# Kernel optimization log

Measured on AMD Instinct MI355X. Metric: run time of the kernel, lower is better.

The kernel has to match this reference:

```python
import jax, jax.numpy as jnp
import numpy as np

EPS = 1e-16


def setup_inputs() -> dict:
    key = jax.random.key(0)
    k1, k2 = jax.random.split(key)
    N, D = 512, 4096
    a = jax.random.normal(k1, (N, D), dtype=jnp.float32)
    p = jax.random.normal(k2, (N, D), dtype=jnp.float32)
    return {"a": a, "p": p}


def reference(a, p):
    N = a.shape[0]
    # Pairwise squared distances between anchors a and positives p:
    # ||a_i||^2 - 2 a_i . p_j + ||p_j||^2   (diag(a a^T) == row norms)
    dot = jnp.matmul(a, p.T)                       # [N, N]
    sq_a = jnp.sum(a * a, axis=-1)                 # [N]
    sq_p = jnp.sum(p * p, axis=-1)                 # [N]
    d2 = sq_a[:, None] - 2.0 * dot + sq_p[None, :]
    d2 = jnp.maximum(d2, 0.0)                      # distances[distances < 0] = 0
    zero_mask = (d2 == 0.0).astype(d2.dtype)
    dist = (1.0 - zero_mask) * jnp.sqrt(d2 + zero_mask * EPS)  # [N, N]

    # Triplet tensor: loss[a, p, n] = dist[a, p] - dist[a, n]
    triplet = dist[:, :, None] - dist[:, None, :]  # [N, N, N]

    # Validity mask: labels = arange(N) -> valid iff p == anchor and n != anchor
    labels = jnp.arange(N)
    label_eq = labels[:, None] == labels[None, :]  # [N, N]
    mask = label_eq[:, :, None] & (~label_eq[:, None, :])  # [N, N, N]

    triplet = mask.astype(triplet.dtype) * triplet
    triplet = jax.nn.relu(triplet)

    num_positive = jnp.sum(triplet > EPS).astype(triplet.dtype)
    loss = jnp.sum(triplet) / (num_positive + EPS)
    return loss
```

## Files before the change

kernel.cpp:

```cpp
#include <hip/hip_runtime.h>
#include <math.h>

#define PN 512
#define PD 4096

#define KSZ 8
#define KCHUNK (PD / KSZ)
#define BK 64
#define NSTAGE (KCHUNK / BK)

#define F_SA 0
#define F_SP 512
#define F_DD 1024
#define F_SUM 1536
#define F_CNT 1537
#define F_DONE 1538
#define F_TILECNT 1600
#define WS_AH_BYTES 8192
#define WS_PH_BYTES (8192 + 4194304)
#define WS_PART_FLOAT 2099200
#define WS_NEED ((size_t)WS_PART_FLOAT * 4 + (size_t)64 * KSZ * 4096 * 4)

typedef __attribute__((ext_vector_type(8))) short short8;
typedef __attribute__((ext_vector_type(4))) float floatx4;

static __device__ __forceinline__ unsigned short f2bf(float x) {
    unsigned int u = __float_as_uint(x);
    u += 0x7fffu + ((u >> 16) & 1u);
    return (unsigned short)(u >> 16);
}

static __device__ __forceinline__ void load16_lds(const void* gp, void* lp) {
    __builtin_amdgcn_global_load_lds(
        (const __attribute__((address_space(1))) unsigned int*)gp,
        (__attribute__((address_space(3))) unsigned int*)lp,
        16, 0, 0);
}

struct ushort4s { unsigned short x, y, z, w; };

__global__ __launch_bounds__(256) void taw_prep_kernel(
        const float* __restrict__ a, const float* __restrict__ p,
        float* __restrict__ ws) {
    const int i = blockIdx.x;
    const int t = threadIdx.x;
    if (i == 0 && t < 128) ((unsigned int*)ws)[1536 + t] = 0u;
    const float4* a4 = (const float4*)(a + (size_t)i * PD);
    const float4* p4 = (const float4*)(p + (size_t)i * PD);
    unsigned short* ah = (unsigned short*)((char*)ws + WS_AH_BYTES) + (size_t)i * PD;
    unsigned short* ph = (unsigned short*)((char*)ws + WS_PH_BYTES) + (size_t)i * PD;
    float sa = 0.f, sp = 0.f, dp = 0.f;
#pragma unroll
    for (int c = 0; c < 4; ++c) {
        const int e = c * 256 + t;
        float4 av = a4[e];
        float4 pv = p4[e];
        sa += av.x * av.x + av.y * av.y + av.z * av.z + av.w * av.w;
        sp += pv.x * pv.x + pv.y * pv.y + pv.z * pv.z + pv.w * pv.w;
        dp += av.x * pv.x + av.y * pv.y + av.z * pv.z + av.w * pv.w;
        ushort4s ab = {f2bf(av.x), f2bf(av.y), f2bf(av.z), f2bf(av.w)};
        ushort4s pb = {f2bf(pv.x), f2bf(pv.y), f2bf(pv.z), f2bf(pv.w)};
        *(ushort4s*)(ah + (size_t)e * 4) = ab;
        *(ushort4s*)(ph + (size_t)e * 4) = pb;
    }
#pragma unroll
    for (int off = 32; off > 0; off >>= 1) {
        sa += __shfl_down(sa, off, 64);
        sp += __shfl_down(sp, off, 64);
        dp += __shfl_down(dp, off, 64);
    }
    __shared__ float red[3][4];
    const int wave = t >> 6;
    if ((t & 63) == 0) { red[0][wave] = sa; red[1][wave] = sp; red[2][wave] = dp; }
    __syncthreads();
    if (t == 0) {
        sa = red[0][0] + red[0][1] + red[0][2] + red[0][3];
        sp = red[1][0] + red[1][1] + red[1][2] + red[1][3];
        dp = red[2][0] + red[2][1] + red[2][2] + red[2][3];
        float d2 = sa - 2.f * dp + sp;
        d2 = fmaxf(d2, 0.f);
        ws[F_SA + i] = sa;
        ws[F_SP + i] = sp;
        ws[F_DD + i] = (d2 == 0.f) ? 0.f : sqrtf(d2);
    }
}

__global__ __launch_bounds__(256) void taw_fused_kernel(float* __restrict__ ws,
                                                        float* __restrict__ out) {
    __shared__ short lds[2][8][64][8];
    const unsigned short* ah = (const unsigned short*)((const char*)ws + WS_AH_BYTES);
    const unsigned short* ph = (const unsigned short*)((const char*)ws + WS_PH_BYTES);
    const int t = threadIdx.x;
    const int lane = t & 63;
    const int w = t >> 6;
    const int wm = w >> 1, wn = w & 1;
    const int i0 = blockIdx.y * 64;
    const int j0 = blockIdx.x * 64;
    const int tile = blockIdx.y * 8 + blockIdx.x;
    const int kzb = blockIdx.z * KCHUNK;
    unsigned int* wsu = (unsigned int*)ws;

    floatx4 acc[2][2] = {{{0.f, 0.f, 0.f, 0.f}, {0.f, 0.f, 0.f, 0.f}},
                         {{0.f, 0.f, 0.f, 0.f}, {0.f, 0.f, 0.f, 0.f}}};

    for (int st = 0; st < NSTAGE; ++st) {
        const int kb = kzb + st * BK;
        __syncthreads();
#pragma unroll
        for (int q = 0; q < 2; ++q) {
            const int g = 2 * w + q;
            const int row = ((g & 3) << 4) + (lane & 15);
            const int kk = kb + ((((g >> 2) << 2) + (lane >> 4)) << 3);
            load16_lds(ah + (size_t)(i0 + row) * PD + kk, &lds[0][g][0][0]);
            load16_lds(ph + (size_t)(j0 + row) * PD + kk, &lds[1][g][0][0]);
        }
        __syncthreads();
#pragma unroll
        for (int s2 = 0; s2 < 2; ++s2) {
            short8 af0 = *(const short8*)&lds[0][s2 * 4 + wm * 2 + 0][lane][0];
            short8 af1 = *(const short8*)&lds[0][s2 * 4 + wm * 2 + 1][lane][0];
            short8 bf0 = *(const short8*)&lds[1][s2 * 4 + wn * 2 + 0][lane][0];
            short8 bf1 = *(const short8*)&lds[1][s2 * 4 + wn * 2 + 1][lane][0];
            acc[0][0] = __builtin_amdgcn_mfma_f32_16x16x32_bf16(af0, bf0, acc[0][0], 0, 0, 0);
            acc[0][1] = __builtin_amdgcn_mfma_f32_16x16x32_bf16(af0, bf1, acc[0][1], 0, 0, 0);
            acc[1][0] = __builtin_amdgcn_mfma_f32_16x16x32_bf16(af1, bf0, acc[1][0], 0, 0, 0);
            acc[1][1] = __builtin_amdgcn_mfma_f32_16x16x32_bf16(af1, bf1, acc[1][1], 0, 0, 0);
        }
    }

    float* part = ws + WS_PART_FLOAT + ((size_t)tile * KSZ + blockIdx.z) * 4096;
    const int jj = wn * 32 + (lane & 15);
    const int ib = wm * 32 + ((lane >> 4) << 2);
#pragma unroll
    for (int rm = 0; rm < 2; ++rm)
#pragma unroll
        for (int rn = 0; rn < 2; ++rn)
#pragma unroll
            for (int r = 0; r < 4; ++r)
                part[(ib + rm * 16 + r) * 64 + jj + rn * 16] = acc[rm][rn][r];

    __syncthreads();
    __shared__ unsigned int lastflag;
    if (t == 0) {
        __threadfence();
        lastflag = (atomicAdd(&wsu[F_TILECNT + tile], 1u) == KSZ - 1) ? 1u : 0u;
    }
    __syncthreads();
    if (!lastflag) return;

    const float* pbase = ws + WS_PART_FLOAT + (size_t)tile * KSZ * 4096;
    const int row = t >> 2;
    const int c0 = (t & 3) * 16;
    const int gi = i0 + row;
    const float sa = ws[F_SA + gi];
    const float dd = ws[F_DD + gi];
    float lsum = 0.f;
    unsigned int lcnt = 0;
#pragma unroll
    for (int v = 0; v < 4; ++v) {
        const int e = row * 64 + c0 + v * 4;
        float4 d = *(const float4*)(pbase + e);
#pragma unroll
        for (int k = 1; k < KSZ; ++k) {
            const float4 q = *(const float4*)(pbase + k * 4096 + e);
            d.x += q.x; d.y += q.y; d.z += q.z; d.w += q.w;
        }
        const int gj = j0 + c0 + v * 4;
        const float4 sp4 = *(const float4*)(ws + F_SP + gj);
        const float dr[4] = {d.x, d.y, d.z, d.w};
        const float sr[4] = {sp4.x, sp4.y, sp4.z, sp4.w};
#pragma unroll
        for (int c = 0; c < 4; ++c) {
            float d2 = sa - 2.f * dr[c] + sr[c];
            d2 = fmaxf(d2, 0.f);
            const float dist = (d2 == 0.f) ? 0.f : sqrtf(d2);
            const float vv = (gi != gj + c) ? fmaxf(dd - dist, 0.f) : 0.f;
            lsum += vv;
            lcnt += (vv > 1e-16f) ? 1u : 0u;
        }
    }
#pragma unroll
    for (int off = 32; off > 0; off >>= 1) {
        lsum += __shfl_down(lsum, off, 64);
        lcnt += __shfl_down(lcnt, off, 64);
    }
    __shared__ float rsum[4];
    __shared__ unsigned int rcnt[4];
    if (lane == 0) { rsum[w] = lsum; rcnt[w] = lcnt; }
    __syncthreads();
    if (t == 0) {
        atomicAdd(ws + F_SUM, rsum[0] + rsum[1] + rsum[2] + rsum[3]);
        atomicAdd(&wsu[F_CNT], rcnt[0] + rcnt[1] + rcnt[2] + rcnt[3]);
        __threadfence();
        if (atomicAdd(&wsu[F_DONE], 1u) == 63u) {
            __threadfence();
            const float s = atomicAdd(ws + F_SUM, 0.0f);
            const unsigned int c = atomicAdd(&wsu[F_CNT], 0u);
            out[0] = (float)((double)s / ((double)c + 1e-16));
        }
    }
}

__global__ __launch_bounds__(256) void taw_gemm_loss_kernel(
        const float* __restrict__ A, const float* __restrict__ P,
        float* __restrict__ ws) {
    __shared__ float as[32][34];
    __shared__ float bs[32][34];
    const int tx = threadIdx.x;
    const int ty = threadIdx.y;
    const int t = ty * 16 + tx;
    const int i0 = blockIdx.y * 32;
    const int j0 = blockIdx.x * 32;
    const int sr = t >> 3;
    const int sk = (t & 7) * 4;
    const float* aptr = A + (size_t)(i0 + sr) * PD + sk;
    const float* pptr = P + (size_t)(j0 + sr) * PD + sk;
    float c00 = 0.f, c01 = 0.f, c10 = 0.f, c11 = 0.f;
    for (int k0 = 0; k0 < PD; k0 += 32) {
        float4 av = *(const float4*)(aptr + k0);
        float4 pv = *(const float4*)(pptr + k0);
        __syncthreads();
        as[sk + 0][sr] = av.x; as[sk + 1][sr] = av.y;
        as[sk + 2][sr] = av.z; as[sk + 3][sr] = av.w;
        bs[sk + 0][sr] = pv.x; bs[sk + 1][sr] = pv.y;
        bs[sk + 2][sr] = pv.z; bs[sk + 3][sr] = pv.w;
        __syncthreads();
#pragma unroll
        for (int kk = 0; kk < 32; ++kk) {
            const float2 a2 = *(const float2*)&as[kk][2 * ty];
            const float2 b2 = *(const float2*)&bs[kk][2 * tx];
            c00 = fmaf(a2.x, b2.x, c00);
            c01 = fmaf(a2.x, b2.y, c01);
            c10 = fmaf(a2.y, b2.x, c10);
            c11 = fmaf(a2.y, b2.y, c11);
        }
    }
    const int i = i0 + 2 * ty;
    const int j = j0 + 2 * tx;
    float cvals[2][2] = {{c00, c01}, {c10, c11}};
    float lsum = 0.f;
    unsigned int lcnt = 0;
#pragma unroll
    for (int dr = 0; dr < 2; ++dr)
#pragma unroll
        for (int dc = 0; dc < 2; ++dc) {
            const int ii = i + dr, jj = j + dc;
            float d2 = ws[F_SA + ii] - 2.f * cvals[dr][dc] + ws[F_SP + jj];
            d2 = fmaxf(d2, 0.f);
            const float dist = (d2 == 0.f) ? 0.f : sqrtf(d2);
            const float v = (ii != jj) ? fmaxf(ws[F_DD + ii] - dist, 0.f) : 0.f;
            lsum += v;
            lcnt += (v > 1e-16f) ? 1u : 0u;
        }
#pragma unroll
    for (int off = 32; off > 0; off >>= 1) {
        lsum += __shfl_down(lsum, off, 64);
        lcnt += __shfl_down(lcnt, off, 64);
    }
    __shared__ float rsum[4];
    __shared__ unsigned int rcnt[4];
    if ((t & 63) == 0) { rsum[t >> 6] = lsum; rcnt[t >> 6] = lcnt; }
    __syncthreads();
    if (t == 0) {
        atomicAdd(ws + F_SUM, rsum[0] + rsum[1] + rsum[2] + rsum[3]);
        atomicAdd(((unsigned int*)ws) + F_CNT, rcnt[0] + rcnt[1] + rcnt[2] + rcnt[3]);
    }
}

__global__ void taw_finalize_kernel(const float* __restrict__ ws,
                                    float* __restrict__ out) {
    const double s = (double)ws[F_SUM];
    const double c = (double)(((const unsigned int*)ws)[F_CNT]);
    out[0] = (float)(s / (c + 1e-16));
}

extern "C" void kernel_launch(void* const* d_in, const int* in_sizes, int n_in,
                              void* d_out, int out_size, void* d_ws, size_t ws_size,
                              hipStream_t stream) {
    (void)in_sizes; (void)n_in; (void)out_size;
    const float* a = (const float*)d_in[0];
    const float* p = (const float*)d_in[1];
    float* out = (float*)d_out;
    float* ws = (float*)d_ws;

    taw_prep_kernel<<<PN, 256, 0, stream>>>(a, p, ws);
    if (ws_size >= WS_NEED) {
        taw_fused_kernel<<<dim3(8, 8, KSZ), 256, 0, stream>>>(ws, out);
    } else {
        taw_gemm_loss_kernel<<<dim3(16, 16), dim3(16, 16), 0, stream>>>(a, p, ws);
        taw_finalize_kernel<<<1, 1, 0, stream>>>(ws, out);
    }
}
```

Before: 97.84 us.

## Replace global split-K partials with in-block split-K over 32x32 tiles

The fused GEMM+loss kernel moves from 64x64 tiles with an 8-way split-K across blocks to 32x32 tiles with 256 blocks of 1024 threads. Each block's 16 waves split K four ways and reduce their partial accumulators through LDS. This removes the global partial buffer, the per-tile atomic counter and the reload of partials by the last block. In exchange each block performs more barriers per stage, each wave issues only two MFMAs per stage, and the larger blocks may lower occupancy.

```diff
diff --git a/kernel.cpp b/kernel.cpp
--- a/kernel.cpp
+++ b/kernel.cpp
@@ -3,11 +3,6 @@
 
 #define PN 512
 #define PD 4096
-
-#define KSZ 8
-#define KCHUNK (PD / KSZ)
-#define BK 64
-#define NSTAGE (KCHUNK / BK)
 
 #define F_SA 0
 #define F_SP 512
@@ -15,11 +10,9 @@
 #define F_SUM 1536
 #define F_CNT 1537
 #define F_DONE 1538
-#define F_TILECNT 1600
 #define WS_AH_BYTES 8192
 #define WS_PH_BYTES (8192 + 4194304)
-#define WS_PART_FLOAT 2099200
-#define WS_NEED ((size_t)WS_PART_FLOAT * 4 + (size_t)64 * KSZ * 4096 * 4)
+#define WS_NEED ((size_t)(8192 + 2 * 4194304))
 
 typedef __attribute__((ext_vector_type(8))) short short8;
 typedef __attribute__((ext_vector_type(4))) float floatx4;
@@ -44,7 +37,7 @@
         float* __restrict__ ws) {
     const int i = blockIdx.x;
     const int t = threadIdx.x;
-    if (i == 0 && t < 128) ((unsigned int*)ws)[1536 + t] = 0u;
+    if (i == 0 && t < 64) ((unsigned int*)ws)[1536 + t] = 0u;
     const float4* a4 = (const float4*)(a + (size_t)i * PD);
     const float4* p4 = (const float4*)(p + (size_t)i * PD);
     unsigned short* ah = (unsigned short*)((char*)ws + WS_AH_BYTES) + (size_t)i * PD;
@@ -85,120 +78,95 @@
     }
 }
 
-__global__ __launch_bounds__(256) void taw_fused_kernel(float* __restrict__ ws,
-                                                        float* __restrict__ out) {
-    __shared__ short lds[2][8][64][8];
+__global__ __launch_bounds__(1024) void taw_fused_kernel(float* __restrict__ ws,
+                                                         float* __restrict__ out) {
+    __shared__ __attribute__((aligned(16))) char shraw[32768];
+    short* sbase = (short*)shraw;
+    float* rbase = (float*)shraw;
     const unsigned short* ah = (const unsigned short*)((const char*)ws + WS_AH_BYTES);
     const unsigned short* ph = (const unsigned short*)((const char*)ws + WS_PH_BYTES);
+    unsigned int* wsu = (unsigned int*)ws;
+
     const int t = threadIdx.x;
     const int lane = t & 63;
     const int w = t >> 6;
-    const int wm = w >> 1, wn = w & 1;
-    const int i0 = blockIdx.y * 64;
-    const int j0 = blockIdx.x * 64;
-    const int tile = blockIdx.y * 8 + blockIdx.x;
-    const int kzb = blockIdx.z * KCHUNK;
-    unsigned int* wsu = (unsigned int*)ws;
-
-    floatx4 acc[2][2] = {{{0.f, 0.f, 0.f, 0.f}, {0.f, 0.f, 0.f, 0.f}},
-                         {{0.f, 0.f, 0.f, 0.f}, {0.f, 0.f, 0.f, 0.f}}};
-
-    for (int st = 0; st < NSTAGE; ++st) {
-        const int kb = kzb + st * BK;
-        __syncthreads();
-#pragma unroll
-        for (int q = 0; q < 2; ++q) {
-            const int g = 2 * w + q;
-            const int row = ((g & 3) << 4) + (lane & 15);
-            const int kk = kb + ((((g >> 2) << 2) + (lane >> 4)) << 3);
-            load16_lds(ah + (size_t)(i0 + row) * PD + kk, &lds[0][g][0][0]);
-            load16_lds(ph + (size_t)(j0 + row) * PD + kk, &lds[1][g][0][0]);
-        }
-        __syncthreads();
-#pragma unroll
-        for (int s2 = 0; s2 < 2; ++s2) {
-            short8 af0 = *(const short8*)&lds[0][s2 * 4 + wm * 2 + 0][lane][0];
-            short8 af1 = *(const short8*)&lds[0][s2 * 4 + wm * 2 + 1][lane][0];
-            short8 bf0 = *(const short8*)&lds[1][s2 * 4 + wn * 2 + 0][lane][0];
-            short8 bf1 = *(const short8*)&lds[1][s2 * 4 + wn * 2 + 1][lane][0];
-            acc[0][0] = __builtin_amdgcn_mfma_f32_16x16x32_bf16(af0, bf0, acc[0][0], 0, 0, 0);
-            acc[0][1] = __builtin_amdgcn_mfma_f32_16x16x32_bf16(af0, bf1, acc[0][1], 0, 0, 0);
-            acc[1][0] = __builtin_amdgcn_mfma_f32_16x16x32_bf16(af1, bf0, acc[1][0], 0, 0, 0);
-            acc[1][1] = __builtin_amdgcn_mfma_f32_16x16x32_bf16(af1, bf1, acc[1][1], 0, 0, 0);
-        }
-    }
-
-    float* part = ws + WS_PART_FLOAT + ((size_t)tile * KSZ + blockIdx.z) * 4096;
-    const int jj = wn * 32 + (lane & 15);
-    const int ib = wm * 32 + ((lane >> 4) << 2);
-#pragma unroll
-    for (int rm = 0; rm < 2; ++rm)
-#pragma unroll
-        for (int rn = 0; rn < 2; ++rn)
-#pragma unroll
-            for (int r = 0; r < 4; ++r)
-                part[(ib + rm * 16 + r) * 64 + jj + rn * 16] = acc[rm][rn][r];
-
-    __syncthreads();
-    __shared__ unsigned int lastflag;
-    if (t == 0) {
-        __threadfence();
-        lastflag = (atomicAdd(&wsu[F_TILECNT + tile], 1u) == KSZ - 1) ? 1u : 0u;
-    }
-    __syncthreads();
-    if (!lastflag) return;
-
-    const float* pbase = ws + WS_PART_FLOAT + (size_t)tile * KSZ * 4096;
-    const int row = t >> 2;
-    const int c0 = (t & 3) * 16;
-    const int gi = i0 + row;
-    const float sa = ws[F_SA + gi];
-    const float dd = ws[F_DD + gi];
-    float lsum = 0.f;
-    unsigned int lcnt = 0;
-#pragma unroll
-    for (int v = 0; v < 4; ++v) {
-        const int e = row * 64 + c0 + v * 4;
-        float4 d = *(const float4*)(pbase + e);
-#pragma unroll
-        for (int k = 1; k < KSZ; ++k) {
-            const float4 q = *(const float4*)(pbase + k * 4096 + e);
-            d.x += q.x; d.y += q.y; d.z += q.z; d.w += q.w;
-        }
-        const int gj = j0 + c0 + v * 4;
-        const float4 sp4 = *(const float4*)(ws + F_SP + gj);
-        const float dr[4] = {d.x, d.y, d.z, d.w};
-        const float sr[4] = {sp4.x, sp4.y, sp4.z, sp4.w};
-#pragma unroll
-        for (int c = 0; c < 4; ++c) {
-            float d2 = sa - 2.f * dr[c] + sr[c];
+    const int kg = w >> 2;
+    const int quad = w & 3;
+    const int qm = quad >> 1, qn = quad & 1;
+    const int i0 = blockIdx.y * 32;
+    const int j0 = blockIdx.x * 32;
+    const int kgbase = kg << 10;
+
+#define SG_OFF(KG, ARR, G) (((((KG) * 2 + (ARR)) * 4) + (G)) * 512)
+
+    const int lrow = ((quad & 1) << 4) + (lane & 15);
+    const int lkof = ((quad >> 1) << 5) + ((lane >> 4) << 3);
+    const unsigned short* agp = ah + (size_t)(i0 + lrow) * PD + kgbase + lkof;
+    const unsigned short* pgp = ph + (size_t)(j0 + lrow) * PD + kgbase + lkof;
+    short* sA = sbase + SG_OFF(kg, 0, quad);
+    short* sB = sbase + SG_OFF(kg, 1, quad);
+
+    floatx4 acc = {0.f, 0.f, 0.f, 0.f};
+    const int lane8 = lane * 8;
+
+    for (int st = 0; st < 16; ++st) {
+        __syncthreads();
+        load16_lds(agp + st * 64, sA);
+        load16_lds(pgp + st * 64, sB);
+        __syncthreads();
+        short8 af0 = *(const short8*)(sbase + SG_OFF(kg, 0, qm) + lane8);
+        short8 bf0 = *(const short8*)(sbase + SG_OFF(kg, 1, qn) + lane8);
+        short8 af1 = *(const short8*)(sbase + SG_OFF(kg, 0, 2 + qm) + lane8);
+        short8 bf1 = *(const short8*)(sbase + SG_OFF(kg, 1, 2 + qn) + lane8);
+        acc = __builtin_amdgcn_mfma_f32_16x16x32_bf16(af0, bf0, acc, 0, 0, 0);
+        acc = __builtin_amdgcn_mfma_f32_16x16x32_bf16(af1, bf1, acc, 0, 0, 0);
+    }
+
+    __syncthreads();
+    *(floatx4*)(rbase + (((kg * 4 + quad) * 64) + lane) * 4) = acc;
+    __syncthreads();
+
+    __shared__ float rs[4];
+    __shared__ unsigned int rc[4];
+    if (kg == 0) {
+        floatx4 d = *(const floatx4*)(rbase + (((0 * 4 + quad) * 64) + lane) * 4);
+#pragma unroll
+        for (int k = 1; k < 4; ++k)
+            d += *(const floatx4*)(rbase + (((k * 4 + quad) * 64) + lane) * 4);
+        const int gj = j0 + qn * 16 + (lane & 15);
+        const float spj = ws[F_SP + gj];
+        float lsum = 0.f;
+        unsigned int lcnt = 0;
+#pragma unroll
+        for (int r = 0; r < 4; ++r) {
+            const int gi = i0 + qm * 16 + ((lane >> 4) << 2) + r;
+            float d2 = ws[F_SA + gi] - 2.f * d[r] + spj;
             d2 = fmaxf(d2, 0.f);
             const float dist = (d2 == 0.f) ? 0.f : sqrtf(d2);
-            const float vv = (gi != gj + c) ? fmaxf(dd - dist, 0.f) : 0.f;
-            lsum += vv;
-            lcnt += (vv > 1e-16f) ? 1u : 0u;
-        }
-    }
-#pragma unroll
-    for (int off = 32; off > 0; off >>= 1) {
-        lsum += __shfl_down(lsum, off, 64);
-        lcnt += __shfl_down(lcnt, off, 64);
-    }
-    __shared__ float rsum[4];
-    __shared__ unsigned int rcnt[4];
-    if (lane == 0) { rsum[w] = lsum; rcnt[w] = lcnt; }
+            const float v = (gi != gj) ? fmaxf(ws[F_DD + gi] - dist, 0.f) : 0.f;
+            lsum += v;
+            lcnt += (v > 1e-16f) ? 1u : 0u;
+        }
+#pragma unroll
+        for (int off = 32; off > 0; off >>= 1) {
+            lsum += __shfl_down(lsum, off, 64);
+            lcnt += __shfl_down(lcnt, off, 64);
+        }
+        if (lane == 0) { rs[quad] = lsum; rc[quad] = lcnt; }
+    }
     __syncthreads();
     if (t == 0) {
-        atomicAdd(ws + F_SUM, rsum[0] + rsum[1] + rsum[2] + rsum[3]);
-        atomicAdd(&wsu[F_CNT], rcnt[0] + rcnt[1] + rcnt[2] + rcnt[3]);
+        atomicAdd(ws + F_SUM, rs[0] + rs[1] + rs[2] + rs[3]);
+        atomicAdd(&wsu[F_CNT], rc[0] + rc[1] + rc[2] + rc[3]);
         __threadfence();
-        if (atomicAdd(&wsu[F_DONE], 1u) == 63u) {
+        if (atomicAdd(&wsu[F_DONE], 1u) == 255u) {
             __threadfence();
             const float s = atomicAdd(ws + F_SUM, 0.0f);
             const unsigned int c = atomicAdd(&wsu[F_CNT], 0u);
             out[0] = (float)((double)s / ((double)c + 1e-16));
         }
     }
+#undef SG_OFF
 }
 
 __global__ __launch_bounds__(256) void taw_gemm_loss_kernel(
@@ -285,7 +253,7 @@
 
     taw_prep_kernel<<<PN, 256, 0, stream>>>(a, p, ws);
     if (ws_size >= WS_NEED) {
-        taw_fused_kernel<<<dim3(8, 8, KSZ), 256, 0, stream>>>(ws, out);
+        taw_fused_kernel<<<dim3(16, 16), 1024, 0, stream>>>(ws, out);
     } else {
         taw_gemm_loss_kernel<<<dim3(16, 16), dim3(16, 16), 0, stream>>>(a, p, ws);
         taw_finalize_kernel<<<1, 1, 0, stream>>>(ws, out);
```

New measurement: 98.52 us. No clear change (+0.7%).
